# Optimization experiments

Hardware: AMD Instinct MI355X
Metric: run time of the kernel (lower is better)

The kernel has to match this reference:

```python
import jax, jax.numpy as jnp
import numpy as np

B, T, D, F_FF, E, K = 8, 2048, 1024, 4096, 8, 2


def setup_inputs() -> dict:
    key = jax.random.key(0)
    ks = jax.random.split(key, 6)
    s = 1.0 / np.sqrt(D)
    return {
        "x": jax.random.normal(ks[0], (B, T, D), jnp.float32),
        "Wr": jax.random.normal(ks[1], (D, E), jnp.float32) * s,
        "W1": jax.random.normal(ks[2], (E, D, F_FF), jnp.float32) * s,
        "b1": jax.random.normal(ks[3], (E, F_FF), jnp.float32) * 0.01,
        "W2": jax.random.normal(ks[4], (E, F_FF, D), jnp.float32) * (1.0 / np.sqrt(F_FF)),
        "b2": jax.random.normal(ks[5], (E, D), jnp.float32) * 0.01,
    }


def reference(x, Wr, W1, b1, W2, b2):
    # Per-SAMPLE routing (matches original: top_idx is (B, K), whole sequence
    # x[b] is processed by the selected expert, scaled by scalar weights[b,k]).
    pooled = x.mean(axis=1)                       # (B, D)
    logits = pooled @ Wr                          # (B, E)
    top_scores, top_idx = jax.lax.top_k(logits, K)  # (B, K)
    weights = jax.nn.softmax(top_scores, axis=-1)   # (B, K)

    # Gather each selected expert's FFN params: (B, K, ...)
    W1s, b1s = W1[top_idx], b1[top_idx]
    W2s, b2s = W2[top_idx], b2[top_idx]

    h = jnp.einsum('btd,bkdf->bktf', x, W1s) + b1s[:, :, None, :]
    h = jax.nn.gelu(h, approximate=False)         # torch F.gelu default = erf
    y = jnp.einsum('bktf,bkfd->bktd', h, W2s) + b2s[:, :, None, :]
    out = jnp.einsum('bk,bktd->btd', weights, y)  # weighted combine
    return out
```

## Files before the change

### kernel.cpp

```cpp
#include <hip/hip_runtime.h>

#define T_SEQ 2048
#define DDIM  1024
#define FDIM  4096
#define NE    8

typedef __attribute__((ext_vector_type(8))) __bf16 bf16x8;
typedef __attribute__((ext_vector_type(4))) float  f32x4;

__device__ __forceinline__ void gld16(const void* g, void* l) {
    __builtin_amdgcn_global_load_lds(
        (__attribute__((address_space(1))) void*)g,
        (__attribute__((address_space(3))) void*)l,
        16, 0, 0);
}

__global__ void kpool(const float* __restrict__ x, float* __restrict__ part) {
    int bd = blockIdx.x * 256 + threadIdx.x;
    int tc = blockIdx.y;
    int b = bd >> 10;
    int d = bd & 1023;
    const float* p = x + ((size_t)b * T_SEQ + (size_t)tc * 256) * DDIM + d;
    float s = 0.f;
    #pragma unroll 8
    for (int t = 0; t < 256; ++t) s += p[(size_t)t * DDIM];
    part[tc * 8192 + bd] = s;
}

__global__ void kroute(const float* __restrict__ part, const float* __restrict__ Wr,
                       int* __restrict__ ridx, float* __restrict__ rw) {
    __shared__ float pooled[8192];
    __shared__ float plg[256];
    __shared__ float lg[64];
    int tid = threadIdx.x;
    for (int i = tid; i < 8192; i += 256) {
        float s = 0.f;
        #pragma unroll
        for (int tc = 0; tc < 8; ++tc) s += part[tc * 8192 + i];
        pooled[i] = s * (1.0f / (float)T_SEQ);
    }
    __syncthreads();
    {
        int b = tid >> 5, e = (tid >> 2) & 7, q = tid & 3;
        float s = 0.f;
        const float* pb = pooled + b * 1024 + q * 256;
        for (int d = 0; d < 256; ++d) s += pb[d] * Wr[(q * 256 + d) * NE + e];
        plg[tid] = s;
    }
    __syncthreads();
    if (tid < 64) {
        int b = tid >> 3, e = tid & 7;
        int base = b * 32 + e * 4;
        lg[tid] = plg[base] + plg[base + 1] + plg[base + 2] + plg[base + 3];
    }
    __syncthreads();
    if (tid < 8) {
        int b = tid;
        float best = -1e30f; int bi = 0;
        #pragma unroll
        for (int e = 0; e < 8; ++e) { float v = lg[b * 8 + e]; if (v > best) { best = v; bi = e; } }
        float best2 = -1e30f; int bi2 = 0;
        #pragma unroll
        for (int e = 0; e < 8; ++e) {
            if (e == bi) continue;
            float v = lg[b * 8 + e];
            if (v > best2) { best2 = v; bi2 = e; }
        }
        float e1 = __expf(best2 - best);
        float inv = 1.0f / (1.0f + e1);
        ridx[b * 2]     = bi;
        ridx[b * 2 + 1] = bi2;
        rw[b * 2]     = inv;
        rw[b * 2 + 1] = e1 * inv;
    }
}

__global__ void kconvX(const float* __restrict__ in, __bf16* __restrict__ out) {
    size_t i = ((size_t)blockIdx.x * 256 + threadIdx.x) * 4;
    float4 v = *(const float4*)(in + i);
    union { __bf16 h[4]; uint2 u; } pk;
    pk.h[0] = (__bf16)v.x; pk.h[1] = (__bf16)v.y;
    pk.h[2] = (__bf16)v.z; pk.h[3] = (__bf16)v.w;
    *(uint2*)(out + i) = pk.u;
}

__global__ void kconvT(const float* __restrict__ in, __bf16* __restrict__ out,
                       int R, int C) {
    __shared__ float t[64][65];
    int e  = blockIdx.z;
    int r0 = blockIdx.y * 64;
    int c0 = blockIdx.x * 64;
    int tid = threadIdx.x;
    const float* ip = in + ((size_t)e * R + r0) * C + c0;
    int tr  = tid >> 4;
    int tc4 = (tid & 15) * 4;
    #pragma unroll
    for (int j = 0; j < 4; ++j) {
        float4 v = *(const float4*)(ip + (size_t)(tr + j * 16) * C + tc4);
        t[tr + j * 16][tc4 + 0] = v.x;
        t[tr + j * 16][tc4 + 1] = v.y;
        t[tr + j * 16][tc4 + 2] = v.z;
        t[tr + j * 16][tc4 + 3] = v.w;
    }
    __syncthreads();
    __bf16* op = out + ((size_t)e * C + c0) * R + r0;
    int oc  = tid >> 2;
    int orb = (tid & 3) * 16;
    #pragma unroll
    for (int s = 0; s < 4; ++s) {
        int orr = orb + s * 4;
        union { __bf16 h[4]; uint2 u; } pk;
        pk.h[0] = (__bf16)t[orr + 0][oc];
        pk.h[1] = (__bf16)t[orr + 1][oc];
        pk.h[2] = (__bf16)t[orr + 2][oc];
        pk.h[3] = (__bf16)t[orr + 3][oc];
        *(uint2*)(op + (size_t)oc * R + orr) = pk.u;
    }
}

template<int K>
__device__ __forceinline__ void mma256(
    const __bf16* __restrict__ A, const __bf16* __restrict__ B,
    __bf16* __restrict__ lds,
    f32x4 (&acc)[8][4], int m0, int n0)
{
    constexpr int nt = K >> 6;
    const int tid = threadIdx.x;
    const int l  = tid & 63;
    const int w  = tid >> 6;
    const int lr = l & 15;
    const int lq = l >> 4;
    const int wm = w >> 2;
    const int wn = w & 3;

    long aoff[2], boff[2];
    int  lA[2],  lB[2];
    #pragma unroll
    for (int j = 0; j < 2; ++j) {
        aoff[j] = (long)(m0 + (w << 4) + lr) * K + (j << 5) + (lq << 3);
        boff[j] = (long)(n0 + (w << 4) + lr) * K + (j << 5) + (lq << 3);
        lA[j] = (2 * w + j) * 512 + l * 8;
        lB[j] = 16384 + (2 * w + j) * 512 + l * 8;
    }
    const long rhalf = (long)128 * K;

    const int afo = wm * 8 * 1024 + l * 8;
    const int bfo = 16384 + wn * 4 * 1024 + l * 8;

    #pragma unroll
    for (int j = 0; j < 2; ++j) {
        gld16(A + aoff[j],         lds + lA[j]);
        gld16(A + aoff[j] + rhalf, lds + lA[j] + 8192);
        gld16(B + boff[j],         lds + lB[j]);
        gld16(B + boff[j] + rhalf, lds + lB[j] + 8192);
    }
    if (nt > 1) {
        __bf16* d1 = lds + 32768;
        #pragma unroll
        for (int j = 0; j < 2; ++j) {
            gld16(B + boff[j] + 64,         d1 + lB[j]);
            gld16(B + boff[j] + rhalf + 64, d1 + lB[j] + 8192);
        }
        asm volatile("s_waitcnt vmcnt(4)" ::: "memory");
    } else {
        asm volatile("s_waitcnt vmcnt(0)" ::: "memory");
    }
    __builtin_amdgcn_s_barrier();

    bf16x8 bfr[4][2];
    for (int t = 0; t < nt; ++t) {
        const __bf16* cur = lds + (t & 1) * 32768;
        __bf16* nx1 = lds + ((t + 1) & 1) * 32768;
        __bf16* nx2 = lds + (t & 1) * 32768;
        const long ko1 = (long)(t + 1) << 6;
        const long ko2 = (long)(t + 2) << 6;

        bf16x8 af[2][2];

        #pragma unroll
        for (int kk = 0; kk < 2; ++kk) {
            af[0][kk] = *(const bf16x8*)(cur + afo + 0 * 1024 + kk * 512);
            af[1][kk] = *(const bf16x8*)(cur + afo + 1 * 1024 + kk * 512);
            #pragma unroll
            for (int jn = 0; jn < 4; ++jn)
                bfr[jn][kk] = *(const bf16x8*)(cur + bfo + jn * 1024 + kk * 512);
        }
        if (t + 1 < nt) {
            #pragma unroll
            for (int j = 0; j < 2; ++j)
                gld16(A + aoff[j] + ko1, nx1 + lA[j]);
        }
        __builtin_amdgcn_s_barrier();
        asm volatile("s_waitcnt lgkmcnt(0)" ::: "memory");
        __builtin_amdgcn_sched_barrier(0);
        __builtin_amdgcn_s_setprio(1);
        #pragma unroll
        for (int kk = 0; kk < 2; ++kk)
            #pragma unroll
            for (int jn = 0; jn < 4; ++jn) {
                acc[0][jn] = __builtin_amdgcn_mfma_f32_16x16x32_bf16(af[0][kk], bfr[jn][kk], acc[0][jn], 0, 0, 0);
                acc[1][jn] = __builtin_amdgcn_mfma_f32_16x16x32_bf16(af[1][kk], bfr[jn][kk], acc[1][jn], 0, 0, 0);
            }
        __builtin_amdgcn_s_setprio(0);
        __builtin_amdgcn_s_barrier();

        #pragma unroll
        for (int kk = 0; kk < 2; ++kk) {
            af[0][kk] = *(const bf16x8*)(cur + afo + 2 * 1024 + kk * 512);
            af[1][kk] = *(const bf16x8*)(cur + afo + 3 * 1024 + kk * 512);
        }
        if (t + 1 < nt) {
            #pragma unroll
            for (int j = 0; j < 2; ++j)
                gld16(A + aoff[j] + rhalf + ko1, nx1 + lA[j] + 8192);
        }
        __builtin_amdgcn_s_barrier();
        asm volatile("s_waitcnt lgkmcnt(0)" ::: "memory");
        __builtin_amdgcn_sched_barrier(0);
        __builtin_amdgcn_s_setprio(1);
        #pragma unroll
        for (int kk = 0; kk < 2; ++kk)
            #pragma unroll
            for (int jn = 0; jn < 4; ++jn) {
                acc[2][jn] = __builtin_amdgcn_mfma_f32_16x16x32_bf16(af[0][kk], bfr[jn][kk], acc[2][jn], 0, 0, 0);
                acc[3][jn] = __builtin_amdgcn_mfma_f32_16x16x32_bf16(af[1][kk], bfr[jn][kk], acc[3][jn], 0, 0, 0);
            }
        __builtin_amdgcn_s_setprio(0);
        __builtin_amdgcn_s_barrier();

        #pragma unroll
        for (int kk = 0; kk < 2; ++kk) {
            af[0][kk] = *(const bf16x8*)(cur + afo + 4 * 1024 + kk * 512);
            af[1][kk] = *(const bf16x8*)(cur + afo + 5 * 1024 + kk * 512);
        }
        if (t + 2 < nt) {
            #pragma unroll
            for (int j = 0; j < 2; ++j)
                gld16(B + boff[j] + ko2, nx2 + lB[j]);
        }
        __builtin_amdgcn_s_barrier();
        asm volatile("s_waitcnt lgkmcnt(0)" ::: "memory");
        __builtin_amdgcn_sched_barrier(0);
        __builtin_amdgcn_s_setprio(1);
        #pragma unroll
        for (int kk = 0; kk < 2; ++kk)
            #pragma unroll
            for (int jn = 0; jn < 4; ++jn) {
                acc[4][jn] = __builtin_amdgcn_mfma_f32_16x16x32_bf16(af[0][kk], bfr[jn][kk], acc[4][jn], 0, 0, 0);
                acc[5][jn] = __builtin_amdgcn_mfma_f32_16x16x32_bf16(af[1][kk], bfr[jn][kk], acc[5][jn], 0, 0, 0);
            }
        __builtin_amdgcn_s_setprio(0);
        __builtin_amdgcn_s_barrier();

        #pragma unroll
        for (int kk = 0; kk < 2; ++kk) {
            af[0][kk] = *(const bf16x8*)(cur + afo + 6 * 1024 + kk * 512);
            af[1][kk] = *(const bf16x8*)(cur + afo + 7 * 1024 + kk * 512);
        }
        if (t + 2 < nt) {
            #pragma unroll
            for (int j = 0; j < 2; ++j)
                gld16(B + boff[j] + rhalf + ko2, nx2 + lB[j] + 8192);
        }
        __builtin_amdgcn_s_barrier();
        asm volatile("s_waitcnt lgkmcnt(0)" ::: "memory");
        __builtin_amdgcn_sched_barrier(0);
        __builtin_amdgcn_s_setprio(1);
        #pragma unroll
        for (int kk = 0; kk < 2; ++kk)
            #pragma unroll
            for (int jn = 0; jn < 4; ++jn) {
                acc[6][jn] = __builtin_amdgcn_mfma_f32_16x16x32_bf16(af[0][kk], bfr[jn][kk], acc[6][jn], 0, 0, 0);
                acc[7][jn] = __builtin_amdgcn_mfma_f32_16x16x32_bf16(af[1][kk], bfr[jn][kk], acc[7][jn], 0, 0, 0);
            }
        __builtin_amdgcn_s_setprio(0);
        if (t + 1 < nt) {
            if (t + 2 < nt) asm volatile("s_waitcnt vmcnt(4)" ::: "memory");
            else            asm volatile("s_waitcnt vmcnt(0)" ::: "memory");
        }
        __builtin_amdgcn_s_barrier();
    }
}

__global__ __launch_bounds__(512, 2) void gemm1_kernel(
    const __bf16* __restrict__ xbf, const __bf16* __restrict__ W1t,
    const float* __restrict__ b1, const int* __restrict__ ridx,
    const float* __restrict__ rw, __bf16* __restrict__ h, int p0)
{
    __shared__ __attribute__((aligned(16))) __bf16 lds[65536];
    const int lp = blockIdx.z;
    const int p  = p0 + lp;
    const int b  = p >> 1;
    const int e  = ridx[p];
    const float wgt = rw[p];
    const int m0 = blockIdx.y * 256;
    const int n0 = blockIdx.x * 256;

    f32x4 acc[8][4];
    #pragma unroll
    for (int i = 0; i < 8; ++i)
        #pragma unroll
        for (int j = 0; j < 4; ++j)
            acc[i][j] = (f32x4){0.f, 0.f, 0.f, 0.f};

    mma256<DDIM>(xbf + (size_t)b * T_SEQ * DDIM, W1t + (size_t)e * FDIM * DDIM,
                 lds, acc, m0, n0);

    const int l  = threadIdx.x & 63;
    const int w  = threadIdx.x >> 6;
    const int wmo = (w >> 2) << 7, wno = (w & 3) << 6;
    const int lr = l & 15, lq = l >> 4;
    __bf16* hd = h + (size_t)lp * T_SEQ * FDIM;
    const float* bias = b1 + e * FDIM;
    #pragma unroll
    for (int im = 0; im < 8; ++im) {
        int row = m0 + wmo + im * 16 + lq * 4;
        #pragma unroll
        for (int jn = 0; jn < 4; ++jn) {
            int col = n0 + wno + jn * 16 + lr;
            float bv = bias[col];
            #pragma unroll
            for (int r = 0; r < 4; ++r) {
                float v = acc[im][jn][r] + bv;
                v = 0.5f * v * (1.0f + erff(v * 0.70710678118654752f));
                hd[(size_t)(row + r) * FDIM + col] = (__bf16)(wgt * v);
            }
        }
    }
}

__global__ __launch_bounds__(512, 2) void gemm2_kernel(
    const __bf16* __restrict__ h, const __bf16* __restrict__ W2t,
    const float* __restrict__ b2, const int* __restrict__ ridx,
    const float* __restrict__ rw, float* __restrict__ out, int s0)
{
    __shared__ __attribute__((aligned(16))) __bf16 lds[65536];
    const int ls = blockIdx.z;
    const int s  = s0 + ls;
    const int e0 = ridx[s * 2], e1 = ridx[s * 2 + 1];
    const float w0 = rw[s * 2], w1 = rw[s * 2 + 1];
    const int m0 = blockIdx.y * 256;
    const int n0 = blockIdx.x * 256;

    f32x4 acc[8][4];
    #pragma unroll
    for (int i = 0; i < 8; ++i)
        #pragma unroll
        for (int j = 0; j < 4; ++j)
            acc[i][j] = (f32x4){0.f, 0.f, 0.f, 0.f};

    mma256<FDIM>(h + (size_t)(2 * ls) * T_SEQ * FDIM, W2t + (size_t)e0 * DDIM * FDIM,
                 lds, acc, m0, n0);
    mma256<FDIM>(h + (size_t)(2 * ls + 1) * T_SEQ * FDIM, W2t + (size_t)e1 * DDIM * FDIM,
                 lds, acc, m0, n0);

    const int l  = threadIdx.x & 63;
    const int w  = threadIdx.x >> 6;
    const int wmo = (w >> 2) << 7, wno = (w & 3) << 6;
    const int lr = l & 15, lq = l >> 4;
    float* od = out + (size_t)s * T_SEQ * DDIM;
    const float* bb0 = b2 + e0 * DDIM;
    const float* bb1 = b2 + e1 * DDIM;
    #pragma unroll
    for (int im = 0; im < 8; ++im) {
        int row = m0 + wmo + im * 16 + lq * 4;
        #pragma unroll
        for (int jn = 0; jn < 4; ++jn) {
            int col = n0 + wno + jn * 16 + lr;
            float bv = w0 * bb0[col] + w1 * bb1[col];
            #pragma unroll
            for (int r = 0; r < 4; ++r)
                od[(size_t)(row + r) * DDIM + col] = acc[im][jn][r] + bv;
        }
    }
}

extern "C" void kernel_launch(void* const* d_in, const int* in_sizes, int n_in,
                              void* d_out, int out_size, void* d_ws, size_t ws_size,
                              hipStream_t stream) {
    const float* x  = (const float*)d_in[0];
    const float* Wr = (const float*)d_in[1];
    const float* W1 = (const float*)d_in[2];
    const float* b1 = (const float*)d_in[3];
    const float* W2 = (const float*)d_in[4];
    const float* b2 = (const float*)d_in[5];
    float* out = (float*)d_out;
    char*  ws  = (char*)d_ws;

    int*    ridx = (int*)(ws + 0);
    float*  rw   = (float*)(ws + 64);
    float*  part = (float*)(ws + 1024);
    __bf16* xbf  = (__bf16*)(ws + ((size_t)1  << 20));
    __bf16* W1t  = (__bf16*)(ws + ((size_t)33 << 20));
    __bf16* W2t  = (__bf16*)(ws + ((size_t)97 << 20));
    __bf16* hbuf = (__bf16*)(ws + ((size_t)161 << 20));

    kpool <<<dim3(32, 8), 256, 0, stream>>>(x, part);
    kroute<<<1, 256, 0, stream>>>(part, Wr, ridx, rw);
    kconvX<<<16384, 256, 0, stream>>>(x, xbf);
    kconvT<<<dim3(FDIM / 64, DDIM / 64, NE), 256, 0, stream>>>(W1, W1t, DDIM, FDIM);
    kconvT<<<dim3(DDIM / 64, FDIM / 64, NE), 256, 0, stream>>>(W2, W2t, FDIM, DDIM);

    const size_t h_per_sample = (size_t)2 * T_SEQ * FDIM * sizeof(__bf16);
    size_t hcap = (ws_size > ((size_t)161 << 20)) ? ws_size - ((size_t)161 << 20) : 0;
    int csmax = (int)(hcap / h_per_sample);
    if (csmax < 1) csmax = 1;
    if (csmax > 8) csmax = 8;

    for (int smp0 = 0; smp0 < 8; smp0 += csmax) {
        int cs = (8 - smp0 < csmax) ? (8 - smp0) : csmax;
        gemm1_kernel<<<dim3(FDIM / 256, T_SEQ / 256, 2 * cs), 512, 0, stream>>>(
            xbf, W1t, b1, ridx, rw, hbuf, smp0 * 2);
        gemm2_kernel<<<dim3(DDIM / 256, T_SEQ / 256, cs), 512, 0, stream>>>(
            hbuf, W2t, b2, ridx, rw, out, smp0);
    }
}
```

Measured before the change: 1.072 ms.

## Swizzle GEMM block order across XCDs and reorder MFMA fragment loads per K-half

The GEMM grids become 1D launches, and each block index is remapped so that consecutive tiles sharing the same weight and activation panels land on the same XCD, which should improve L2 reuse. The inner loop is also restructured to load four A fragments per phase and split the B fragments by K-half rather than loading all B up front. This spreads LDS reads more evenly across the four MFMA phases. The swizzle assumes the grid size is divisible by 8 and relies on the fixed tile-count bit decoding.

Result: no change. 1.060 ms (-1.1%).

```diff
diff --git a/kernel.cpp b/kernel.cpp
--- a/kernel.cpp
+++ b/kernel.cpp
@@ -13,6 +13,11 @@
         (__attribute__((address_space(1))) void*)g,
         (__attribute__((address_space(3))) void*)l,
         16, 0, 0);
+}
+
+__device__ __forceinline__ int xcd_swz(int bid, int nblk) {
+    int chunk = nblk >> 3;
+    return (bid & 7) * chunk + (bid >> 3);
 }
 
 __global__ void kpool(const float* __restrict__ x, float* __restrict__ part) {
@@ -175,16 +180,14 @@
         const long ko1 = (long)(t + 1) << 6;
         const long ko2 = (long)(t + 2) << 6;
 
-        bf16x8 af[2][2];
-
-        #pragma unroll
-        for (int kk = 0; kk < 2; ++kk) {
-            af[0][kk] = *(const bf16x8*)(cur + afo + 0 * 1024 + kk * 512);
-            af[1][kk] = *(const bf16x8*)(cur + afo + 1 * 1024 + kk * 512);
-            #pragma unroll
-            for (int jn = 0; jn < 4; ++jn)
-                bfr[jn][kk] = *(const bf16x8*)(cur + bfo + jn * 1024 + kk * 512);
-        }
+        bf16x8 af[4];
+
+        #pragma unroll
+        for (int i = 0; i < 4; ++i)
+            af[i] = *(const bf16x8*)(cur + afo + i * 1024);
+        #pragma unroll
+        for (int jn = 0; jn < 4; ++jn)
+            bfr[jn][0] = *(const bf16x8*)(cur + bfo + jn * 1024);
         if (t + 1 < nt) {
             #pragma unroll
             for (int j = 0; j < 2; ++j)
@@ -195,20 +198,19 @@
         __builtin_amdgcn_sched_barrier(0);
         __builtin_amdgcn_s_setprio(1);
         #pragma unroll
-        for (int kk = 0; kk < 2; ++kk)
-            #pragma unroll
-            for (int jn = 0; jn < 4; ++jn) {
-                acc[0][jn] = __builtin_amdgcn_mfma_f32_16x16x32_bf16(af[0][kk], bfr[jn][kk], acc[0][jn], 0, 0, 0);
-                acc[1][jn] = __builtin_amdgcn_mfma_f32_16x16x32_bf16(af[1][kk], bfr[jn][kk], acc[1][jn], 0, 0, 0);
-            }
+        for (int i = 0; i < 4; ++i)
+            #pragma unroll
+            for (int jn = 0; jn < 4; ++jn)
+                acc[i][jn] = __builtin_amdgcn_mfma_f32_16x16x32_bf16(af[i], bfr[jn][0], acc[i][jn], 0, 0, 0);
         __builtin_amdgcn_s_setprio(0);
         __builtin_amdgcn_s_barrier();
 
         #pragma unroll
-        for (int kk = 0; kk < 2; ++kk) {
-            af[0][kk] = *(const bf16x8*)(cur + afo + 2 * 1024 + kk * 512);
-            af[1][kk] = *(const bf16x8*)(cur + afo + 3 * 1024 + kk * 512);
-        }
+        for (int i = 0; i < 4; ++i)
+            af[i] = *(const bf16x8*)(cur + afo + (4 + i) * 1024);
+        #pragma unroll
+        for (int jn = 0; jn < 4; ++jn)
+            bfr[jn][1] = *(const bf16x8*)(cur + bfo + jn * 1024 + 512);
         if (t + 1 < nt) {
             #pragma unroll
             for (int j = 0; j < 2; ++j)
@@ -219,20 +221,16 @@
         __builtin_amdgcn_sched_barrier(0);
         __builtin_amdgcn_s_setprio(1);
         #pragma unroll
-        for (int kk = 0; kk < 2; ++kk)
-            #pragma unroll
-            for (int jn = 0; jn < 4; ++jn) {
-                acc[2][jn] = __builtin_amdgcn_mfma_f32_16x16x32_bf16(af[0][kk], bfr[jn][kk], acc[2][jn], 0, 0, 0);
-                acc[3][jn] = __builtin_amdgcn_mfma_f32_16x16x32_bf16(af[1][kk], bfr[jn][kk], acc[3][jn], 0, 0, 0);
-            }
+        for (int i = 0; i < 4; ++i)
+            #pragma unroll
+            for (int jn = 0; jn < 4; ++jn)
+                acc[4 + i][jn] = __builtin_amdgcn_mfma_f32_16x16x32_bf16(af[i], bfr[jn][0], acc[4 + i][jn], 0, 0, 0);
         __builtin_amdgcn_s_setprio(0);
         __builtin_amdgcn_s_barrier();
 
         #pragma unroll
-        for (int kk = 0; kk < 2; ++kk) {
-            af[0][kk] = *(const bf16x8*)(cur + afo + 4 * 1024 + kk * 512);
-            af[1][kk] = *(const bf16x8*)(cur + afo + 5 * 1024 + kk * 512);
-        }
+        for (int i = 0; i < 4; ++i)
+            af[i] = *(const bf16x8*)(cur + afo + i * 1024 + 512);
         if (t + 2 < nt) {
             #pragma unroll
             for (int j = 0; j < 2; ++j)
@@ -243,20 +241,16 @@
         __builtin_amdgcn_sched_barrier(0);
         __builtin_amdgcn_s_setprio(1);
         #pragma unroll
-        for (int kk = 0; kk < 2; ++kk)
-            #pragma unroll
-            for (int jn = 0; jn < 4; ++jn) {
-                acc[4][jn] = __builtin_amdgcn_mfma_f32_16x16x32_bf16(af[0][kk], bfr[jn][kk], acc[4][jn], 0, 0, 0);
-                acc[5][jn] = __builtin_amdgcn_mfma_f32_16x16x32_bf16(af[1][kk], bfr[jn][kk], acc[5][jn], 0, 0, 0);
-            }
+        for (int i = 0; i < 4; ++i)
+            #pragma unroll
+            for (int jn = 0; jn < 4; ++jn)
+                acc[i][jn] = __builtin_amdgcn_mfma_f32_16x16x32_bf16(af[i], bfr[jn][1], acc[i][jn], 0, 0, 0);
         __builtin_amdgcn_s_setprio(0);
         __builtin_amdgcn_s_barrier();
 
         #pragma unroll
-        for (int kk = 0; kk < 2; ++kk) {
-            af[0][kk] = *(const bf16x8*)(cur + afo + 6 * 1024 + kk * 512);
-            af[1][kk] = *(const bf16x8*)(cur + afo + 7 * 1024 + kk * 512);
-        }
+        for (int i = 0; i < 4; ++i)
+            af[i] = *(const bf16x8*)(cur + afo + (4 + i) * 1024 + 512);
         if (t + 2 < nt) {
             #pragma unroll
             for (int j = 0; j < 2; ++j)
@@ -267,12 +261,10 @@
         __builtin_amdgcn_sched_barrier(0);
         __builtin_amdgcn_s_setprio(1);
         #pragma unroll
-        for (int kk = 0; kk < 2; ++kk)
-            #pragma unroll
-            for (int jn = 0; jn < 4; ++jn) {
-                acc[6][jn] = __builtin_amdgcn_mfma_f32_16x16x32_bf16(af[0][kk], bfr[jn][kk], acc[6][jn], 0, 0, 0);
-                acc[7][jn] = __builtin_amdgcn_mfma_f32_16x16x32_bf16(af[1][kk], bfr[jn][kk], acc[7][jn], 0, 0, 0);
-            }
+        for (int i = 0; i < 4; ++i)
+            #pragma unroll
+            for (int jn = 0; jn < 4; ++jn)
+                acc[4 + i][jn] = __builtin_amdgcn_mfma_f32_16x16x32_bf16(af[i], bfr[jn][1], acc[4 + i][jn], 0, 0, 0);
         __builtin_amdgcn_s_setprio(0);
         if (t + 1 < nt) {
             if (t + 2 < nt) asm volatile("s_waitcnt vmcnt(4)" ::: "memory");
@@ -288,13 +280,16 @@
     const float* __restrict__ rw, __bf16* __restrict__ h, int p0)
 {
     __shared__ __attribute__((aligned(16))) __bf16 lds[65536];
-    const int lp = blockIdx.z;
+    const int sb = xcd_swz(blockIdx.x, gridDim.x);
+    const int bx = sb & 15;
+    const int by = (sb >> 4) & 7;
+    const int lp = sb >> 7;
     const int p  = p0 + lp;
     const int b  = p >> 1;
     const int e  = ridx[p];
     const float wgt = rw[p];
-    const int m0 = blockIdx.y * 256;
-    const int n0 = blockIdx.x * 256;
+    const int m0 = by * 256;
+    const int n0 = bx * 256;
 
     f32x4 acc[8][4];
     #pragma unroll
@@ -335,12 +330,15 @@
     const float* __restrict__ rw, float* __restrict__ out, int s0)
 {
     __shared__ __attribute__((aligned(16))) __bf16 lds[65536];
-    const int ls = blockIdx.z;
+    const int sb = xcd_swz(blockIdx.x, gridDim.x);
+    const int bx = sb & 3;
+    const int by = (sb >> 2) & 7;
+    const int ls = sb >> 5;
     const int s  = s0 + ls;
     const int e0 = ridx[s * 2], e1 = ridx[s * 2 + 1];
     const float w0 = rw[s * 2], w1 = rw[s * 2 + 1];
-    const int m0 = blockIdx.y * 256;
-    const int n0 = blockIdx.x * 256;
+    const int m0 = by * 256;
+    const int n0 = bx * 256;
 
     f32x4 acc[8][4];
     #pragma unroll
@@ -409,9 +407,9 @@
 
     for (int smp0 = 0; smp0 < 8; smp0 += csmax) {
         int cs = (8 - smp0 < csmax) ? (8 - smp0) : csmax;
-        gemm1_kernel<<<dim3(FDIM / 256, T_SEQ / 256, 2 * cs), 512, 0, stream>>>(
+        gemm1_kernel<<<16 * 8 * 2 * cs, 512, 0, stream>>>(
             xbf, W1t, b1, ridx, rw, hbuf, smp0 * 2);
-        gemm2_kernel<<<dim3(DDIM / 256, T_SEQ / 256, cs), 512, 0, stream>>>(
+        gemm2_kernel<<<4 * 8 * cs, 512, 0, stream>>>(
             hbuf, W2t, b2, ridx, rw, out, smp0);
     }
 }
```
